# Kernel optimization log

Hardware: AMD Instinct MI355X
Metric: run time of the kernel (lower is better)

The kernel has to match this reference:

```python
import jax, jax.numpy as jnp
import numpy as np

N_NODES = 100000
N_EDGES = 1600000
N_GRAPHS = 128
IN_DIM, HID, OUT_DIM, DOC_DIM = 64, 128, 32, 768
LAYERS = 3


def setup_inputs() -> dict:
    key = jax.random.key(0)
    ks = jax.random.split(key, 24)
    s = 0.05
    inp = {
        "x": jax.random.normal(ks[0], (N_NODES, IN_DIM), jnp.float32),
        "doc_features": jax.random.normal(ks[1], (N_GRAPHS, DOC_DIM), jnp.float32),
        "edge_index": jax.random.randint(ks[2], (2, N_EDGES), 0, N_NODES, jnp.int64),
        "batch": jnp.sort(jax.random.randint(ks[3], (N_NODES,), 0, N_GRAPHS, jnp.int64)),
        # parameters (stored as [in, out] so y = x @ W + b)
        "node_w": jax.random.normal(ks[4], (IN_DIM, HID), jnp.float32) * s,
        "node_b": jnp.zeros((HID,), jnp.float32),
        "ggnn_w": jax.random.normal(ks[5], (LAYERS, HID, HID), jnp.float32) * s,
        "gru_w_ih": jax.random.normal(ks[6], (HID, 3 * HID), jnp.float32) * s,
        "gru_b_ih": jnp.zeros((3 * HID,), jnp.float32),
        "gru_w_hh": jax.random.normal(ks[7], (HID, 3 * HID), jnp.float32) * s,
        "gru_b_hh": jnp.zeros((3 * HID,), jnp.float32),
        "doc_w": jax.random.normal(ks[8], (DOC_DIM, HID), jnp.float32) * s,
        "doc_b": jnp.zeros((HID,), jnp.float32),
        "ln_g": jnp.ones((2 * HID,), jnp.float32),
        "ln_b": jnp.zeros((2 * HID,), jnp.float32),
        "fus_w": jax.random.normal(ks[9], (2 * HID, HID), jnp.float32) * s,
        "fus_b": jnp.zeros((HID,), jnp.float32),
        "task_w": jax.random.normal(ks[10], (HID, OUT_DIM), jnp.float32) * s,
        "task_b": jnp.zeros((OUT_DIM,), jnp.float32),
        "time_w": jax.random.normal(ks[11], (HID, 1), jnp.float32) * s,
        "time_b": jnp.zeros((1,), jnp.float32),
    }
    return inp


def _gru(m, h, w_ih, b_ih, w_hh, b_hh):
    gi = m @ w_ih + b_ih  # [N, 3H]
    gh = h @ w_hh + b_hh
    ir, iz, in_ = jnp.split(gi, 3, axis=-1)
    hr, hz, hn = jnp.split(gh, 3, axis=-1)
    r = jax.nn.sigmoid(ir + hr)
    z = jax.nn.sigmoid(iz + hz)
    n = jnp.tanh(in_ + r * hn)
    return (1.0 - z) * n + z * h


def reference(x, doc_features, node_w, node_b, ggnn_w, gru_w_ih, gru_b_ih,
              gru_w_hh, gru_b_hh, doc_w, doc_b, ln_g, ln_b, fus_w, fus_b,
              task_w, task_b, time_w, time_b, edge_index, batch):
    N = x.shape[0]
    src, dst = edge_index[0], edge_index[1]
    # node projection + ReLU
    h = jax.nn.relu(x @ node_w + node_b)  # [N, H]
    # GatedGraphConv: 3 layers of (linear -> scatter-add over edges -> GRU)
    for i in range(LAYERS):
        m = h @ ggnn_w[i]                              # [N, H]
        agg = jax.ops.segment_sum(m[src], dst, num_segments=N)  # scatter-add
        h = _gru(agg, h, gru_w_ih, gru_b_ih, gru_w_hh, gru_b_hh)
    # global mean pool over graphs
    sums = jax.ops.segment_sum(h, batch, num_segments=N_GRAPHS)  # [G, H]
    cnt = jax.ops.segment_sum(jnp.ones((N,), h.dtype), batch, num_segments=N_GRAPHS)
    pooled = sums / jnp.maximum(cnt, 1.0)[:, None]
    # doc projection + fusion head
    doc_emb = jax.nn.relu(doc_features @ doc_w + doc_b)  # [G, H]
    fusion = jnp.concatenate([pooled, doc_emb], axis=1)  # [G, 2H]
    mu = jnp.mean(fusion, axis=-1, keepdims=True)
    var = jnp.mean(jnp.square(fusion - mu), axis=-1, keepdims=True)
    fusion = (fusion - mu) * jax.lax.rsqrt(var + 1e-5) * ln_g + ln_b
    fusion = jax.nn.relu(fusion @ fus_w + fus_b)  # dropout is identity (eval)
    task_output = fusion @ task_w + task_b
    time_output = fusion @ time_w + time_b
    return (task_output, time_output)
```

## Files before the change

### kernel.cpp

```cpp
#include <hip/hip_runtime.h>

#define N_NODES  100000
#define N_EDGES  1600000
#define N_GRAPHS 128
#define SCAN_BLOCKS 98

typedef unsigned short u16;
typedef unsigned int   u32;
typedef __attribute__((ext_vector_type(8))) short short8;
typedef __attribute__((ext_vector_type(4))) float f32x4;

__device__ __forceinline__ float bf2f(u16 v) {
  union { u32 i; float f; } u; u.i = ((u32)v) << 16; return u.f;
}
__device__ __forceinline__ u16 f2bf(float f) {
  union { float f; u32 i; } u; u.f = f;
  u32 r = (u.i + 0x7fffu + ((u.i >> 16) & 1u)) >> 16;
  return (u16)r;
}
__device__ __forceinline__ float sigmoid_f(float x) { return 1.f / (1.f + __expf(-x)); }
__device__ __forceinline__ float tanh_f(float x) {
  x = fminf(15.f, fmaxf(-15.f, x));
  float e = __expf(2.f * x);
  return (e - 1.f) / (e + 1.f);
}
__device__ __forceinline__ int geti(const int* __restrict__ p, int i, int is64) {
  return p[is64 ? (2 * i) : i];
}

__global__ void detect_i64_kernel(const int* __restrict__ ei, const int* __restrict__ batch,
                                  int* __restrict__ flags) {
  int lane = threadIdx.x;
  {
    long long q = (long long)lane * (3200000 / 2 - 1) / 63;
    int pos = (int)(2 * q + 1);
    unsigned long long m = __ballot(ei[pos] != 0);
    if (lane == 0) flags[0] = (m == 0ull) ? 1 : 0;
  }
  {
    long long q = (long long)lane * (100000 / 2 - 1) / 63;
    int pos = (int)(2 * q + 1);
    unsigned long long m = __ballot(batch[pos] != 0);
    if (lane == 0) flags[1] = (m == 0ull) ? 1 : 0;
  }
}

__global__ void hist_kernel(const int* __restrict__ ei, const int* __restrict__ flags,
                            int* __restrict__ counts, u16* __restrict__ rankb) {
  int e = blockIdx.x * 256 + threadIdx.x;
  if (e < N_EDGES) {
    int f = flags[0];
    int d = geti(ei, N_EDGES + e, f);
    int r = atomicAdd(&counts[d], 1);
    rankb[e] = (u16)r;
  }
}

__global__ __launch_bounds__(1024)
void scanA_kernel(const int* __restrict__ counts, int* __restrict__ blocksums) {
  __shared__ int red[16];
  int i = blockIdx.x * 1024 + threadIdx.x;
  int v = (i < N_NODES) ? counts[i] : 0;
  for (int o = 32; o > 0; o >>= 1) v += __shfl_down(v, o, 64);
  int wv = threadIdx.x >> 6, lane = threadIdx.x & 63;
  if (lane == 0) red[wv] = v;
  __syncthreads();
  if (threadIdx.x < 16) {
    int s = red[threadIdx.x];
    for (int o = 8; o > 0; o >>= 1) s += __shfl_down(s, o, 64);
    if (threadIdx.x == 0) blocksums[blockIdx.x] = s;
  }
}

__global__ void scanB_kernel(const int* __restrict__ blocksums, int* __restrict__ blockbase,
                             int* __restrict__ offsets) {
  if (threadIdx.x == 0) {
    int run = 0;
    for (int b = 0; b < SCAN_BLOCKS; ++b) { blockbase[b] = run; run += blocksums[b]; }
    offsets[N_NODES] = run;
  }
}

__global__ __launch_bounds__(1024)
void scanC_kernel(const int* __restrict__ counts, const int* __restrict__ blockbase,
                  int* __restrict__ offsets) {
  __shared__ int buf[1024];
  int t = threadIdx.x;
  int i = blockIdx.x * 1024 + t;
  int v = (i < N_NODES) ? counts[i] : 0;
  buf[t] = v;
  __syncthreads();
  for (int o = 1; o < 1024; o <<= 1) {
    int add = (t >= o) ? buf[t - o] : 0;
    __syncthreads();
    buf[t] += add;
    __syncthreads();
  }
  if (i < N_NODES) offsets[i] = buf[t] - v + blockbase[blockIdx.x];
}

__global__ void scatter_kernel(const int* __restrict__ ei, const int* __restrict__ flags,
                               const int* __restrict__ offsets, const u16* __restrict__ rankb,
                               int* __restrict__ ssrc) {
  int e = blockIdx.x * 256 + threadIdx.x;
  if (e < N_EDGES) {
    int f = flags[0];
    int d = geti(ei, N_EDGES + e, f);
    ssrc[offsets[d] + (int)rankb[e]] = geti(ei, e, f);
  }
}

__global__ void transpose_kernel(const float* __restrict__ in, u16* __restrict__ out, int K, int N) {
  int i = blockIdx.x * 256 + threadIdx.x;
  if (i < K * N) {
    int k = i / N, n = i % N;
    out[n * K + k] = f2bf(in[i]);
  }
}

__global__ void wprime_kernel(const float* __restrict__ ggnn_w, const float* __restrict__ w_ih,
                              float* __restrict__ wp) {
  int i = blockIdx.x * 256 + threadIdx.x;
  if (i >= 3 * 128 * 384) return;
  int l = i / (128 * 384), r = i % (128 * 384), k = r / 384, c = r % 384;
  const float* W = ggnn_w + l * 128 * 128;
  float s = 0.f;
  for (int j = 0; j < 128; ++j) s += W[k * 128 + j] * w_ih[j * 384 + c];
  wp[i] = s;
}

__global__ void build_b2p_kernel(const float* __restrict__ wp, const float* __restrict__ w_hh,
                                 u16* __restrict__ b2p) {
  int g = blockIdx.x * 256 + threadIdx.x;
  if (g >= 8 * 1536 * 8) return;
  int e = g & 7;
  int grp = g >> 3;
  int ci = grp / 1536;
  int idx = grp % 1536;
  int n_lin = idx % 384;
  int ko = idx / 384;
  int k = ci * 32 + ko * 8 + e;
  float v = (k < 128) ? wp[k * 384 + n_lin] : w_hh[(k - 128) * 384 + n_lin];
  b2p[g] = f2bf(v);
}

__global__ __launch_bounds__(256)
void nodeproj_gemm(const float* __restrict__ A, const u16* __restrict__ BT,
                   const float* __restrict__ bias, u16* __restrict__ out, int M)
{
  constexpr int K_DIM = 64, N_DIM = 128, NT = 8, NCHUNK = 2;
  __shared__ u16 B_lds[N_DIM * 40];
  const int tid = threadIdx.x, lane = tid & 63, w = tid >> 6;
  const int strip = blockIdx.x * 64;
  const int ksub = (lane >> 4) * 8;
  union Frag { uint4 u; short8 s; };
  Frag af[NCHUNK];
  const int m_node = strip + w * 16 + (lane & 15);
  const bool avalid = (m_node < M);
#pragma unroll
  for (int ci = 0; ci < NCHUNK; ++ci) {
    int k0 = ci * 32 + ksub;
    short8 sv = {0,0,0,0,0,0,0,0};
    if (avalid) {
      const float* p = A + (size_t)m_node * K_DIM + k0;
      float4 f0 = *(const float4*)p;
      float4 f1 = *(const float4*)(p + 4);
      sv[0]=(short)f2bf(f0.x); sv[1]=(short)f2bf(f0.y); sv[2]=(short)f2bf(f0.z); sv[3]=(short)f2bf(f0.w);
      sv[4]=(short)f2bf(f1.x); sv[5]=(short)f2bf(f1.y); sv[6]=(short)f2bf(f1.z); sv[7]=(short)f2bf(f1.w);
    }
    af[ci].s = sv;
  }
  f32x4 acc[NT];
#pragma unroll
  for (int t = 0; t < NT; ++t) acc[t] = {0.f, 0.f, 0.f, 0.f};
  const int boff = (lane & 15) * 40 + ksub;
#pragma unroll
  for (int ci = 0; ci < NCHUNK; ++ci) {
    if (ci) __syncthreads();
    for (int g = tid; g < N_DIM * 4; g += 256) {
      int n = g >> 2, ko = g & 3;
      uint4 bv = *(const uint4*)(BT + (size_t)n * K_DIM + ci * 32 + ko * 8);
      *(uint4*)(&B_lds[n * 40 + ko * 8]) = bv;
    }
    __syncthreads();
    short8 a = af[ci].s;
#pragma unroll
    for (int t = 0; t < NT; ++t) {
      const short8 b = *(const short8*)(&B_lds[t * 16 * 40 + boff]);
      acc[t] = __builtin_amdgcn_mfma_f32_16x16x32_bf16(a, b, acc[t], 0, 0, 0);
    }
  }
  const int mrow = (lane >> 4) * 4;
#pragma unroll
  for (int t = 0; t < NT; ++t) {
    int col = t * 16 + (lane & 15);
    float bv = bias[col];
#pragma unroll
    for (int r = 0; r < 4; ++r) {
      int node = strip + w * 16 + mrow + r;
      if (node < M) out[(size_t)node * N_DIM + col] = f2bf(fmaxf(acc[t][r] + bv, 0.f));
    }
  }
}

__global__ __launch_bounds__(256)
void gru_gemm(const u16* __restrict__ agg, const u16* __restrict__ h,
              const u16* __restrict__ b2p, const float* __restrict__ b_ih,
              const float* __restrict__ b_hh, u16* __restrict__ hout, int M)
{
  const int tid  = threadIdx.x;
  const int lane = tid & 63;
  const int qc   = tid >> 6;
  const int strip = blockIdx.x * 32;
  const int lrow  = lane & 15;
  const int quad  = lane >> 4;
  const int ksub  = quad * 8;
  if (strip >= M) return;

  f32x4 ar[2][2], az[2][2], ain[2][2], ahn[2][2];
#pragma unroll
  for (int s = 0; s < 2; ++s)
#pragma unroll
    for (int t = 0; t < 2; ++t) {
      ar[s][t] = {0.f,0.f,0.f,0.f}; az[s][t] = {0.f,0.f,0.f,0.f};
      ain[s][t] = {0.f,0.f,0.f,0.f}; ahn[s][t] = {0.f,0.f,0.f,0.f};
    }

  union Frag { uint4 u; short8 s8; };
  const int node0 = strip + lrow;
  const int node1 = strip + 16 + lrow;
  const u16* bb = b2p + ((size_t)quad * 384 + qc * 32 + lrow) * 8;

#pragma unroll
  for (int ci = 0; ci < 8; ++ci) {
    Frag a0, a1;
    {
      const u16* ap = (ci < 4) ? (agg + ci * 32 + ksub) : (h + (ci - 4) * 32 + ksub);
      a0.u = *(const uint4*)(ap + (size_t)node0 * 128);
      a1.u = *(const uint4*)(ap + (size_t)node1 * 128);
    }
    const u16* cb = bb + ci * 12288;
    {
      Frag b[2];
#pragma unroll
      for (int t = 0; t < 2; ++t) b[t].u = *(const uint4*)(cb + t * 128);
#pragma unroll
      for (int t = 0; t < 2; ++t) {
        ar[0][t] = __builtin_amdgcn_mfma_f32_16x16x32_bf16(a0.s8, b[t].s8, ar[0][t], 0, 0, 0);
        ar[1][t] = __builtin_amdgcn_mfma_f32_16x16x32_bf16(a1.s8, b[t].s8, ar[1][t], 0, 0, 0);
      }
    }
    {
      Frag b[2];
#pragma unroll
      for (int t = 0; t < 2; ++t) b[t].u = *(const uint4*)(cb + 1024 + t * 128);
#pragma unroll
      for (int t = 0; t < 2; ++t) {
        az[0][t] = __builtin_amdgcn_mfma_f32_16x16x32_bf16(a0.s8, b[t].s8, az[0][t], 0, 0, 0);
        az[1][t] = __builtin_amdgcn_mfma_f32_16x16x32_bf16(a1.s8, b[t].s8, az[1][t], 0, 0, 0);
      }
    }
    {
      Frag b[2];
#pragma unroll
      for (int t = 0; t < 2; ++t) b[t].u = *(const uint4*)(cb + 2048 + t * 128);
      if (ci < 4) {
#pragma unroll
        for (int t = 0; t < 2; ++t) {
          ain[0][t] = __builtin_amdgcn_mfma_f32_16x16x32_bf16(a0.s8, b[t].s8, ain[0][t], 0, 0, 0);
          ain[1][t] = __builtin_amdgcn_mfma_f32_16x16x32_bf16(a1.s8, b[t].s8, ain[1][t], 0, 0, 0);
        }
      } else {
#pragma unroll
        for (int t = 0; t < 2; ++t) {
          ahn[0][t] = __builtin_amdgcn_mfma_f32_16x16x32_bf16(a0.s8, b[t].s8, ahn[0][t], 0, 0, 0);
          ahn[1][t] = __builtin_amdgcn_mfma_f32_16x16x32_bf16(a1.s8, b[t].s8, ahn[1][t], 0, 0, 0);
        }
      }
    }
  }

#pragma unroll
  for (int t = 0; t < 2; ++t) {
    const int c = qc * 32 + t * 16 + lrow;
    const float brr = b_ih[c] + b_hh[c];
    const float bzz = b_ih[128 + c] + b_hh[128 + c];
    const float bin = b_ih[256 + c];
    const float bhn = b_hh[256 + c];
#pragma unroll
    for (int s = 0; s < 2; ++s) {
#pragma unroll
      for (int r = 0; r < 4; ++r) {
        const int nrow = strip + s * 16 + quad * 4 + r;
        float rg = sigmoid_f(ar[s][t][r] + brr);
        float zg = sigmoid_f(az[s][t][r] + bzz);
        float hv = ahn[s][t][r] + bhn;
        float ng = tanh_f(ain[s][t][r] + bin + rg * hv);
        float hp = bf2f(h[(size_t)nrow * 128 + c]);
        hout[(size_t)nrow * 128 + c] = f2bf((1.f - zg) * ng + zg * hp);
      }
    }
  }
}

__global__ __launch_bounds__(256)
void agg_kernel(const u16* __restrict__ m, const int* __restrict__ ssrc,
                const int* __restrict__ offsets, u16* __restrict__ agg)
{
  int node = blockIdx.x * 4 + (threadIdx.x >> 6);
  int lane = threadIdx.x & 63;
  if (node >= N_NODES) return;
  int beg = offsets[node], end = offsets[node + 1];
  float s0 = 0.f, s1 = 0.f;
  int e = beg;
  for (; e + 8 <= end; e += 8) {
    u32 v[8];
#pragma unroll
    for (int q = 0; q < 8; ++q) {
      int src = ssrc[e + q];
      v[q] = *(const u32*)(m + (size_t)src * 128 + lane * 2);
    }
#pragma unroll
    for (int q = 0; q < 8; ++q) {
      s0 += bf2f((u16)(v[q] & 0xffffu));
      s1 += bf2f((u16)(v[q] >> 16));
    }
  }
  for (; e < end; ++e) {
    int src = ssrc[e];
    u32 v = *(const u32*)(m + (size_t)src * 128 + lane * 2);
    s0 += bf2f((u16)(v & 0xffffu));
    s1 += bf2f((u16)(v >> 16));
  }
  u32 packed = (u32)f2bf(s0) | ((u32)f2bf(s1) << 16);
  *(u32*)(agg + (size_t)node * 128 + lane * 2) = packed;
}

__global__ __launch_bounds__(256)
void pool_kernel(const u16* __restrict__ h, const int* __restrict__ batch,
                 const int* __restrict__ flags, float* __restrict__ sums)
{
  const int c = threadIdx.x & 127;
  const int half = threadIdx.x >> 7;
  const int base = blockIdx.x * 128;
  const int f = flags[1];
  int gcur = -1; float s = 0.f;
  for (int i = half; i < 128; i += 2) {
    int n = base + i;
    if (n >= N_NODES) break;
    int g = geti(batch, n, f);
    if (g != gcur) {
      if (gcur >= 0) atomicAdd(&sums[gcur * 128 + c], s);
      s = 0.f; gcur = g;
    }
    s += bf2f(h[(size_t)n * 128 + c]);
  }
  if (gcur >= 0) atomicAdd(&sums[gcur * 128 + c], s);
}

__global__ __launch_bounds__(256)
void head2_kernel(const float* __restrict__ sums, const int* __restrict__ batch,
                  const int* __restrict__ flags,
                  const float* __restrict__ doc, const float* __restrict__ doc_w, const float* __restrict__ doc_b,
                  const float* __restrict__ ln_g, const float* __restrict__ ln_b,
                  const float* __restrict__ fus_w, const float* __restrict__ fus_b,
                  const float* __restrict__ task_w, const float* __restrict__ task_b,
                  const float* __restrict__ time_w, const float* __restrict__ time_b,
                  float* __restrict__ out_task, float* __restrict__ out_time)
{
  const int g = blockIdx.x;
  const int t = threadIdx.x;
  __shared__ float fusion[256];
  __shared__ float fh[128];
  __shared__ float dpart[256];
  __shared__ int seg[2];

  if (t < 2) {
    int f = flags[1];
    int target = g + t, lo = 0, hi = N_NODES;
    while (lo < hi) { int mid = (lo + hi) >> 1; if (geti(batch, mid, f) < target) lo = mid + 1; else hi = mid; }
    seg[t] = lo;
  }
  {
    int c = t & 127, kh = t >> 7;
    float s = 0.f;
    for (int k = kh * 384; k < kh * 384 + 384; ++k) s += doc[g * 768 + k] * doc_w[k * 128 + c];
    dpart[t] = s;
  }
  __syncthreads();

  if (t < 128) {
    float cnt = (float)(seg[1] - seg[0]);
    fusion[t] = sums[g * 128 + t] / fmaxf(cnt, 1.f);
  } else {
    int c = t - 128;
    fusion[t] = fmaxf(dpart[c] + dpart[c + 128] + doc_b[c], 0.f);
  }
  __syncthreads();

  float mu = 0.f;
  for (int i = 0; i < 256; ++i) mu += fusion[i];
  mu *= (1.f / 256.f);
  float var = 0.f;
  for (int i = 0; i < 256; ++i) { float d = fusion[i] - mu; var += d * d; }
  var *= (1.f / 256.f);
  float inv = rsqrtf(var + 1e-5f);
  float norm = (fusion[t] - mu) * inv * ln_g[t] + ln_b[t];
  __syncthreads();
  fusion[t] = norm;
  __syncthreads();

  if (t < 128) {
    float s = 0.f;
    for (int k = 0; k < 256; ++k) s += fusion[k] * fus_w[k * 128 + t];
    s += fus_b[t];
    fh[t] = fmaxf(s, 0.f);
  }
  __syncthreads();

  if (t < 32) {
    float s = 0.f;
    for (int k = 0; k < 128; ++k) s += fh[k] * task_w[k * 32 + t];
    s += task_b[t];
    out_task[g * 32 + t] = s;
  }
  if (t == 32) {
    float s = 0.f;
    for (int k = 0; k < 128; ++k) s += fh[k] * time_w[k];
    s += time_b[0];
    out_time[g] = s;
  }
}

extern "C" void kernel_launch(void* const* d_in, const int* in_sizes, int n_in,
                              void* d_out, int out_size, void* d_ws, size_t ws_size,
                              hipStream_t stream)
{
  const float* x        = (const float*)d_in[0];
  const float* doc      = (const float*)d_in[1];
  const int*   ei       = (const int*)d_in[2];
  const int*   batch    = (const int*)d_in[3];
  const float* node_w   = (const float*)d_in[4];
  const float* node_b   = (const float*)d_in[5];
  const float* ggnn_w   = (const float*)d_in[6];
  const float* gru_w_ih = (const float*)d_in[7];
  const float* gru_b_ih = (const float*)d_in[8];
  const float* gru_w_hh = (const float*)d_in[9];
  const float* gru_b_hh = (const float*)d_in[10];
  const float* doc_w    = (const float*)d_in[11];
  const float* doc_b    = (const float*)d_in[12];
  const float* ln_g     = (const float*)d_in[13];
  const float* ln_b     = (const float*)d_in[14];
  const float* fus_w    = (const float*)d_in[15];
  const float* fus_b    = (const float*)d_in[16];
  const float* task_w   = (const float*)d_in[17];
  const float* task_b   = (const float*)d_in[18];
  const float* time_w   = (const float*)d_in[19];
  const float* time_b   = (const float*)d_in[20];

  char* ws = (char*)d_ws;
  size_t off = 0;
  auto alloc = [&](size_t bytes) -> void* {
    void* p = ws + off;
    off = (off + bytes + 255) & ~(size_t)255;
    return p;
  };
  u16* aggb   = (u16*)alloc((size_t)N_NODES * 128 * 2);
  u16* hA     = (u16*)alloc((size_t)N_NODES * 128 * 2);
  u16* hB     = (u16*)alloc((size_t)N_NODES * 128 * 2);
  u16* nwT    = (u16*)alloc(64 * 128 * 2);
  u16* b2p    = (u16*)alloc(3 * 8 * 1536 * 8 * 2);
  float* wp   = (float*)alloc(3 * 128 * 384 * 4);
  float* sums = (float*)alloc(N_GRAPHS * 128 * 4);
  int* counts = (int*)alloc((size_t)N_NODES * 4);
  int* offs   = (int*)alloc((size_t)(N_NODES + 1) * 4);
  int* ssrc   = (int*)alloc((size_t)N_EDGES * 4);
  u16* rankb  = (u16*)alloc((size_t)N_EDGES * 2);
  int* bsum   = (int*)alloc(SCAN_BLOCKS * 4);
  int* bbase  = (int*)alloc(SCAN_BLOCKS * 4);
  int* flags  = (int*)alloc(2 * 4);

  hipMemsetAsync(counts, 0, (size_t)N_NODES * 4, stream);
  hipMemsetAsync(sums, 0, (size_t)N_GRAPHS * 128 * 4, stream);

  detect_i64_kernel<<<1, 64, 0, stream>>>(ei, batch, flags);
  hist_kernel<<<(N_EDGES + 255) / 256, 256, 0, stream>>>(ei, flags, counts, rankb);
  scanA_kernel<<<SCAN_BLOCKS, 1024, 0, stream>>>(counts, bsum);
  scanB_kernel<<<1, 64, 0, stream>>>(bsum, bbase, offs);
  scanC_kernel<<<SCAN_BLOCKS, 1024, 0, stream>>>(counts, bbase, offs);
  scatter_kernel<<<(N_EDGES + 255) / 256, 256, 0, stream>>>(ei, flags, offs, rankb, ssrc);

  transpose_kernel<<<(64 * 128 + 255) / 256, 256, 0, stream>>>(node_w, nwT, 64, 128);
  wprime_kernel<<<(3 * 128 * 384 + 255) / 256, 256, 0, stream>>>(ggnn_w, gru_w_ih, wp);
  for (int l = 0; l < 3; ++l)
    build_b2p_kernel<<<(8 * 1536 * 8 + 255) / 256, 256, 0, stream>>>(
        wp + l * 128 * 384, gru_w_hh, b2p + (size_t)l * 8 * 1536 * 8);

  const int GB = (N_NODES + 63) / 64;
  const int GB32 = N_NODES / 32;
  nodeproj_gemm<<<GB, 256, 0, stream>>>(x, nwT, node_b, hA, N_NODES);

  u16* hcur = hA;
  u16* hnext = hB;
  for (int l = 0; l < 3; ++l) {
    agg_kernel<<<(N_NODES + 3) / 4, 256, 0, stream>>>(hcur, ssrc, offs, aggb);
    gru_gemm<<<GB32, 256, 0, stream>>>(aggb, hcur, b2p + (size_t)l * 8 * 1536 * 8,
                                       gru_b_ih, gru_b_hh, hnext, N_NODES);
    u16* tmp = hcur; hcur = hnext; hnext = tmp;
  }

  pool_kernel<<<(N_NODES + 127) / 128, 256, 0, stream>>>(hcur, batch, flags, sums);

  float* out_task = (float*)d_out;
  float* out_time = out_task + N_GRAPHS * 32;
  head2_kernel<<<N_GRAPHS, 256, 0, stream>>>(sums, batch, flags, doc, doc_w, doc_b, ln_g, ln_b,
                                             fus_w, fus_b, task_w, task_b, time_w, time_b,
                                             out_task, out_time);
}
```

Baseline: 717.5 us.

## Double-buffer GRU MFMA operand loads and widen edge-gather loads in aggregation

The GRU MFMA kernel now prefetches the next K-chunk's A and B fragments into a second register buffer while the current chunk's MFMAs run, hiding global load latency. The aggregation kernel changes from one 4-byte load per lane per edge to 16-byte loads, with four lane-groups each handling a different edge and a cross-group shuffle reduction at the end. This cuts the number of load instructions and raises memory-level parallelism in the gather. The cost is higher register pressure in the GRU kernel and extra shuffles plus idle lanes in the aggregation for nodes with few edges.

```diff
diff --git a/kernel.cpp b/kernel.cpp
--- a/kernel.cpp
+++ b/kernel.cpp
@@ -231,51 +231,44 @@
   const int node1 = strip + 16 + lrow;
   const u16* bb = b2p + ((size_t)quad * 384 + qc * 32 + lrow) * 8;
 
+  Frag a0[2], a1[2], fbr[2][2], fbz[2][2], fbg[2][2];
+
+  auto ldchunk = [&](int ci, int p) {
+    const u16* ap = (ci < 4) ? (agg + ci * 32 + ksub) : (h + (ci - 4) * 32 + ksub);
+    a0[p].u = *(const uint4*)(ap + (size_t)node0 * 128);
+    a1[p].u = *(const uint4*)(ap + (size_t)node1 * 128);
+    const u16* cb = bb + ci * 12288;
+    fbr[p][0].u = *(const uint4*)(cb);
+    fbr[p][1].u = *(const uint4*)(cb + 128);
+    fbz[p][0].u = *(const uint4*)(cb + 1024);
+    fbz[p][1].u = *(const uint4*)(cb + 1024 + 128);
+    fbg[p][0].u = *(const uint4*)(cb + 2048);
+    fbg[p][1].u = *(const uint4*)(cb + 2048 + 128);
+  };
+
+  ldchunk(0, 0);
 #pragma unroll
   for (int ci = 0; ci < 8; ++ci) {
-    Frag a0, a1;
-    {
-      const u16* ap = (ci < 4) ? (agg + ci * 32 + ksub) : (h + (ci - 4) * 32 + ksub);
-      a0.u = *(const uint4*)(ap + (size_t)node0 * 128);
-      a1.u = *(const uint4*)(ap + (size_t)node1 * 128);
-    }
-    const u16* cb = bb + ci * 12288;
-    {
-      Frag b[2];
-#pragma unroll
-      for (int t = 0; t < 2; ++t) b[t].u = *(const uint4*)(cb + t * 128);
+    const int p = ci & 1, q = p ^ 1;
+    if (ci < 7) ldchunk(ci + 1, q);
+#pragma unroll
+    for (int t = 0; t < 2; ++t) {
+      ar[0][t] = __builtin_amdgcn_mfma_f32_16x16x32_bf16(a0[p].s8, fbr[p][t].s8, ar[0][t], 0, 0, 0);
+      ar[1][t] = __builtin_amdgcn_mfma_f32_16x16x32_bf16(a1[p].s8, fbr[p][t].s8, ar[1][t], 0, 0, 0);
+      az[0][t] = __builtin_amdgcn_mfma_f32_16x16x32_bf16(a0[p].s8, fbz[p][t].s8, az[0][t], 0, 0, 0);
+      az[1][t] = __builtin_amdgcn_mfma_f32_16x16x32_bf16(a1[p].s8, fbz[p][t].s8, az[1][t], 0, 0, 0);
+    }
+    if (ci < 4) {
 #pragma unroll
       for (int t = 0; t < 2; ++t) {
-        ar[0][t] = __builtin_amdgcn_mfma_f32_16x16x32_bf16(a0.s8, b[t].s8, ar[0][t], 0, 0, 0);
-        ar[1][t] = __builtin_amdgcn_mfma_f32_16x16x32_bf16(a1.s8, b[t].s8, ar[1][t], 0, 0, 0);
+        ain[0][t] = __builtin_amdgcn_mfma_f32_16x16x32_bf16(a0[p].s8, fbg[p][t].s8, ain[0][t], 0, 0, 0);
+        ain[1][t] = __builtin_amdgcn_mfma_f32_16x16x32_bf16(a1[p].s8, fbg[p][t].s8, ain[1][t], 0, 0, 0);
       }
-    }
-    {
-      Frag b[2];
-#pragma unroll
-      for (int t = 0; t < 2; ++t) b[t].u = *(const uint4*)(cb + 1024 + t * 128);
+    } else {
 #pragma unroll
       for (int t = 0; t < 2; ++t) {
-        az[0][t] = __builtin_amdgcn_mfma_f32_16x16x32_bf16(a0.s8, b[t].s8, az[0][t], 0, 0, 0);
-        az[1][t] = __builtin_amdgcn_mfma_f32_16x16x32_bf16(a1.s8, b[t].s8, az[1][t], 0, 0, 0);
-      }
-    }
-    {
-      Frag b[2];
-#pragma unroll
-      for (int t = 0; t < 2; ++t) b[t].u = *(const uint4*)(cb + 2048 + t * 128);
-      if (ci < 4) {
-#pragma unroll
-        for (int t = 0; t < 2; ++t) {
-          ain[0][t] = __builtin_amdgcn_mfma_f32_16x16x32_bf16(a0.s8, b[t].s8, ain[0][t], 0, 0, 0);
-          ain[1][t] = __builtin_amdgcn_mfma_f32_16x16x32_bf16(a1.s8, b[t].s8, ain[1][t], 0, 0, 0);
-        }
-      } else {
-#pragma unroll
-        for (int t = 0; t < 2; ++t) {
-          ahn[0][t] = __builtin_amdgcn_mfma_f32_16x16x32_bf16(a0.s8, b[t].s8, ahn[0][t], 0, 0, 0);
-          ahn[1][t] = __builtin_amdgcn_mfma_f32_16x16x32_bf16(a1.s8, b[t].s8, ahn[1][t], 0, 0, 0);
-        }
+        ahn[0][t] = __builtin_amdgcn_mfma_f32_16x16x32_bf16(a0[p].s8, fbg[p][t].s8, ahn[0][t], 0, 0, 0);
+        ahn[1][t] = __builtin_amdgcn_mfma_f32_16x16x32_bf16(a1[p].s8, fbg[p][t].s8, ahn[1][t], 0, 0, 0);
       }
     }
   }
@@ -310,30 +303,35 @@
   int node = blockIdx.x * 4 + (threadIdx.x >> 6);
   int lane = threadIdx.x & 63;
   if (node >= N_NODES) return;
+  const int g = lane >> 4, l = lane & 15;
   int beg = offsets[node], end = offsets[node + 1];
-  float s0 = 0.f, s1 = 0.f;
-  int e = beg;
-  for (; e + 8 <= end; e += 8) {
-    u32 v[8];
-#pragma unroll
-    for (int q = 0; q < 8; ++q) {
-      int src = ssrc[e + q];
-      v[q] = *(const u32*)(m + (size_t)src * 128 + lane * 2);
-    }
-#pragma unroll
-    for (int q = 0; q < 8; ++q) {
-      s0 += bf2f((u16)(v[q] & 0xffffu));
-      s1 += bf2f((u16)(v[q] >> 16));
-    }
-  }
-  for (; e < end; ++e) {
-    int src = ssrc[e];
-    u32 v = *(const u32*)(m + (size_t)src * 128 + lane * 2);
-    s0 += bf2f((u16)(v & 0xffffu));
-    s1 += bf2f((u16)(v >> 16));
-  }
-  u32 packed = (u32)f2bf(s0) | ((u32)f2bf(s1) << 16);
-  *(u32*)(agg + (size_t)node * 128 + lane * 2) = packed;
+  float s[8] = {0.f,0.f,0.f,0.f,0.f,0.f,0.f,0.f};
+  for (int e = beg; e < end; e += 8) {
+    uint4 v0 = {0u,0u,0u,0u}, v1 = {0u,0u,0u,0u};
+    int e0 = e + g, e1 = e + 4 + g;
+    if (e0 < end) { int src = ssrc[e0]; v0 = *(const uint4*)(m + (size_t)src * 128 + l * 8); }
+    if (e1 < end) { int src = ssrc[e1]; v1 = *(const uint4*)(m + (size_t)src * 128 + l * 8); }
+    u32 w0[4] = {v0.x, v0.y, v0.z, v0.w};
+    u32 w1[4] = {v1.x, v1.y, v1.z, v1.w};
+#pragma unroll
+    for (int i = 0; i < 4; ++i) {
+      s[2*i]   += bf2f((u16)(w0[i] & 0xffffu)) + bf2f((u16)(w1[i] & 0xffffu));
+      s[2*i+1] += bf2f((u16)(w0[i] >> 16))     + bf2f((u16)(w1[i] >> 16));
+    }
+  }
+#pragma unroll
+  for (int i = 0; i < 8; ++i) {
+    s[i] += __shfl_xor(s[i], 16, 64);
+    s[i] += __shfl_xor(s[i], 32, 64);
+  }
+  if (g == 0) {
+    uint4 o;
+    o.x = (u32)f2bf(s[0]) | ((u32)f2bf(s[1]) << 16);
+    o.y = (u32)f2bf(s[2]) | ((u32)f2bf(s[3]) << 16);
+    o.z = (u32)f2bf(s[4]) | ((u32)f2bf(s[5]) << 16);
+    o.w = (u32)f2bf(s[6]) | ((u32)f2bf(s[7]) << 16);
+    *(uint4*)(agg + (size_t)node * 128 + l * 8) = o;
+  }
 }
 
 __global__ __launch_bounds__(256)
```

Measured after the change: 667.4 us. -7.0%, faster.
